# Kernel optimization log

Measured on AMD Instinct MI355X. Metric: run time of the kernel, lower is better.

The kernel has to match this reference:

```python
import jax, jax.numpy as jnp
import numpy as np

PRE_NMS_THRESH = 0.05
PRE_NMS_TOP_N = 1000
NMS_THRESH = 0.6
POST_TOP_N = 100
MIN_SIZE = 0.0


def setup_inputs() -> dict:
    key = jax.random.key(0)
    k1, k2, k3 = jax.random.split(key, 3)
    N, C, H, W = 16, 80, 100, 152
    stride = 8.0
    xs = (jnp.arange(W, dtype=jnp.float32) + 0.5) * stride
    ys = (jnp.arange(H, dtype=jnp.float32) + 0.5) * stride
    yy, xx = jnp.meshgrid(ys, xs, indexing='ij')
    locations = jnp.stack([xx.reshape(-1), yy.reshape(-1)], axis=-1)  # [HW,2] (x,y)
    box_cls = jax.random.normal(k1, (N, C, H, W), jnp.float32) - 2.0  # logits
    box_regression = jax.random.uniform(k2, (N, 4, H, W), jnp.float32) * 64.0  # l,t,r,b >= 0
    centerness = jax.random.normal(k3, (N, 1, H, W), jnp.float32)
    image_sizes = jnp.tile(jnp.array([[800, 1216]], dtype=jnp.int32), (N, 1))  # (h, w)
    return {"locations": locations, "box_cls": box_cls, "box_regression": box_regression,
            "centerness": centerness, "image_sizes": image_sizes}


def _iou_matrix(b):  # b: [K,4] xyxy
    area = (b[:, 2] - b[:, 0]) * (b[:, 3] - b[:, 1])
    lt = jnp.maximum(b[:, None, :2], b[None, :, :2])
    rb = jnp.minimum(b[:, None, 2:], b[None, :, 2:])
    wh = jnp.clip(rb - lt, 0.0)
    inter = wh[..., 0] * wh[..., 1]
    return inter / (area[:, None] + area[None, :] - inter + 1e-9)


def _greedy_nms(iou, valid):  # boxes assumed sorted by score desc
    K = iou.shape[0]
    idx = jnp.arange(K)
    def body(i, sup):
        row = (iou[i] > NMS_THRESH) & (idx > i)
        return jnp.where(sup[i], sup, sup | row)
    sup = jax.lax.fori_loop(0, K, body, ~valid)
    return (~sup) & valid


def _forward(locations, box_cls, box_regression, centerness, image_sizes):
    N, C, H, W = box_cls.shape
    HW = H * W
    cls = jax.nn.sigmoid(jnp.transpose(box_cls, (0, 2, 3, 1)).reshape(N, HW, C))
    reg = jnp.transpose(box_regression, (0, 2, 3, 1)).reshape(N, HW, 4)
    ctr = jax.nn.sigmoid(jnp.transpose(centerness, (0, 2, 3, 1)).reshape(N, HW))
    cand = cls > PRE_NMS_THRESH
    scores = cls * ctr[:, :, None]
    flat = jnp.where(cand, scores, -jnp.inf).reshape(N, HW * C)
    top_scores, top_idx = jax.lax.top_k(flat, PRE_NMS_TOP_N)  # sorted desc
    loc_idx = top_idx // C
    labels = top_idx % C + 1
    valid = top_scores > -jnp.inf
    ar = jnp.arange(N)[:, None]
    reg_k = reg[ar, loc_idx]      # [N,K,4]
    loc_k = locations[loc_idx]    # [N,K,2]
    x1 = loc_k[..., 0] - reg_k[..., 0]
    y1 = loc_k[..., 1] - reg_k[..., 1]
    x2 = loc_k[..., 0] + reg_k[..., 2]
    y2 = loc_k[..., 1] + reg_k[..., 3]
    hi = image_sizes[:, 0:1].astype(x1.dtype)
    wi = image_sizes[:, 1:2].astype(x1.dtype)
    x1 = jnp.clip(x1, 0.0, wi - 1.0); x2 = jnp.clip(x2, 0.0, wi - 1.0)
    y1 = jnp.clip(y1, 0.0, hi - 1.0); y2 = jnp.clip(y2, 0.0, hi - 1.0)
    valid = valid & (x2 - x1 >= MIN_SIZE) & (y2 - y1 >= MIN_SIZE)
    sc = jnp.where(valid, jnp.sqrt(jnp.where(valid, top_scores, 1.0)), 0.0)
    boxes = jnp.stack([x1, y1, x2, y2], axis=-1)  # [N,K,4]
    # multi-class NMS: offset each class into a disjoint coordinate range
    off = labels.astype(x1.dtype) * (jnp.maximum(wi, hi) + 1.0)
    iou = jax.vmap(_iou_matrix)(boxes + off[..., None])  # [N,K,K]
    keep = jax.vmap(_greedy_nms)(iou, valid)
    fscores = jnp.where(keep, sc, -1.0)
    fs, fidx = jax.lax.top_k(fscores, POST_TOP_N)
    fvalid = fs >= 0.0
    boxes_f = boxes[ar, fidx] * fvalid[..., None]
    labels_f = jnp.where(fvalid, labels[ar, fidx], 0)
    dets = jnp.concatenate([boxes_f, jnp.where(fvalid, fs, 0.0)[..., None]], axis=-1)  # [N,100,5]
    return dets, labels_f


def reference(locations, box_cls, box_regression, centerness, image_sizes):
    return _forward(locations, box_cls, box_regression, centerness, image_sizes)
```

## Files before the change

### kernel.cpp

```cpp
#include <hip/hip_runtime.h>
#include <cstdint>

#define NIMG  16
#define NCLS  80
#define HH    100
#define WW    152
#define HWSZ  (HH*WW)
#define HW4   (HWSZ/4)
#define NE    (HWSZ*NCLS)
#define KTOP  1000
#define POSTN 100
#define PRE_T 0.05f
#define NMS_T 0.6f
#define FLOOR_KEY 0x3D000000u
#define FLOOR_BIN 976
#define SEL_CAP   2048
#define NTILE 240
#define NCHUNK (NCLS*NTILE)
#define NSL1  20
#define NSL2  8
#define SCAP  2048
#define MSLICE 16

#define OFF_H1S   0u
#define OFF_H2S   2621440u
#define OFF_CANDS 3670016u
#define OFF_CCNT  5767168u
#define OFF_CMAX  5767680u
#define OFF_BOX   6996480u
#define OFF_SC    7252480u
#define OFF_LAB   7316480u
#define OFF_MASK  7380480u
#define OFF_COLS  9428480u
#define OFF_META  9559552u

__device__ __forceinline__ float sigm(float x) { return 1.f / (1.f + expf(-x)); }

__device__ __forceinline__ uint64_t shfl64(uint64_t v, int src) {
  int lo = __shfl((int)(uint32_t)(v & 0xffffffffu), src, 64);
  int hi = __shfl((int)(uint32_t)(v >> 32), src, 64);
  return ((uint64_t)(uint32_t)hi << 32) | (uint32_t)lo;
}
__device__ __forceinline__ uint64_t shfl64x(uint64_t v, int d) {
  int lo = __shfl_xor((int)(uint32_t)(v & 0xffffffffu), d, 64);
  int hi = __shfl_xor((int)(uint32_t)(v >> 32), d, 64);
  return ((uint64_t)(uint32_t)hi << 32) | (uint32_t)lo;
}

__device__ __forceinline__ void bitonic_desc_tpp(uint64_t* s, int nn, int t, int nt) {
  const int np = nn >> 1;
  for (int k2 = 2; k2 <= nn; k2 <<= 1) {
    for (int j = k2 >> 1; j > 0; j >>= 1) {
      __syncthreads();
      for (int q = t; q < np; q += nt) {
        int i = ((q & ~(j - 1)) << 1) | (q & (j - 1));
        int p = i | j;
        uint64_t a = s[i], b = s[p];
        bool desc = ((i & k2) == 0);
        bool sw = desc ? (a < b) : (a > b);
        if (sw) { s[i] = b; s[p] = a; }
      }
    }
  }
  __syncthreads();
}

__device__ __forceinline__ void findbin_par(
    const unsigned* __restrict__ hsum, unsigned K, int floorbin, int t,
    unsigned* wtot , int* binmax , unsigned* cumAb ,
    int* bin_out, unsigned* cumAbove_out) {
  const int lane = t & 63, w = t >> 6;
  const unsigned b0 = hsum[4 * t + 0], b1 = hsum[4 * t + 1];
  const unsigned b2 = hsum[4 * t + 2], b3 = hsum[4 * t + 3];
  unsigned s = b0 + b1 + b2 + b3;
#pragma unroll
  for (int d = 1; d < 64; d <<= 1) {
    unsigned o = (unsigned)__shfl_down((int)s, d, 64);
    if (lane + d < 64) s += o;
  }
  if (lane == 0) wtot[w] = s;
  if (t == 0) *binmax = -1;
  __syncthreads();
  unsigned wafter = 0;
#pragma unroll
  for (int w2 = 1; w2 < 16; ++w2) if (w + w2 < 16) wafter += wtot[w + w2];
  const unsigned s0 = s + wafter;
  const unsigned s1 = s0 - b0;
  const unsigned s2 = s1 - b1;
  const unsigned s3 = s2 - b2;
  int cand = -1;
  if (s3 >= K) cand = 4 * t + 3;
  else if (s2 >= K) cand = 4 * t + 2;
  else if (s1 >= K) cand = 4 * t + 1;
  else if (s0 >= K) cand = 4 * t + 0;
  if (cand >= 0) atomicMax(binmax, cand);
  __syncthreads();
  const int bin = *binmax;
  const int target = (bin >= 0) ? bin : floorbin;
  if (t == (target >> 2)) {
    unsigned suf = ((target & 3) == 0) ? s0 : ((target & 3) == 1) ? s1
                 : ((target & 3) == 2) ? s2 : s3;
    *cumAb = suf - hsum[target];
  }
  __syncthreads();
  *bin_out = target;
  *cumAbove_out = *cumAb;
}

__global__ void __launch_bounds__(1024) k_hist(
    const float4* __restrict__ cls4, const float4* __restrict__ ctr4,
    unsigned short* __restrict__ h1s, unsigned* __restrict__ cmax) {
  __shared__ unsigned h[4096];
  const int n = blockIdx.x, z = blockIdx.y;
  const int t = threadIdx.x;
  for (int i = t; i < 4096; i += 1024) h[i] = 0;
  __syncthreads();
  const float4* cp = cls4 + (size_t)n * (NE / 4);
  const float4* cr = ctr4 + (size_t)n * HW4;
#pragma unroll
  for (int it = 0; it < 4; ++it) {
    const int idx4 = it * 1024 + t;
    const bool val = idx4 < HW4;
    float ct0 = 0, ct1 = 0, ct2 = 0, ct3 = 0;
    if (val) {
      float4 c4 = cr[idx4];
      ct0 = sigm(c4.x); ct1 = sigm(c4.y); ct2 = sigm(c4.z); ct3 = sigm(c4.w);
    }
    const int tile = idx4 >> 4;
    for (int c = z * 4; c < z * 4 + 4; ++c) {
      unsigned k0 = 0, k1 = 0, k2 = 0, k3 = 0;
      if (val) {
        float4 v = cp[c * HW4 + idx4];
        float s0 = sigm(v.x), s1 = sigm(v.y), s2 = sigm(v.z), s3 = sigm(v.w);
        k0 = (s0 > PRE_T) ? __float_as_uint(s0 * ct0) : 0u;
        k1 = (s1 > PRE_T) ? __float_as_uint(s1 * ct1) : 0u;
        k2 = (s2 > PRE_T) ? __float_as_uint(s2 * ct2) : 0u;
        k3 = (s3 > PRE_T) ? __float_as_uint(s3 * ct3) : 0u;
        if (k0 >= FLOOR_KEY) atomicAdd(&h[k0 >> 20], 1u);
        if (k1 >= FLOOR_KEY) atomicAdd(&h[k1 >> 20], 1u);
        if (k2 >= FLOOR_KEY) atomicAdd(&h[k2 >> 20], 1u);
        if (k3 >= FLOOR_KEY) atomicAdd(&h[k3 >> 20], 1u);
      }
      unsigned km = max(max(k0, k1), max(k2, k3));
      km = max(km, (unsigned)__shfl_xor((int)km, 1, 64));
      km = max(km, (unsigned)__shfl_xor((int)km, 2, 64));
      km = max(km, (unsigned)__shfl_xor((int)km, 4, 64));
      km = max(km, (unsigned)__shfl_xor((int)km, 8, 64));
      if ((t & 15) == 0 && tile < NTILE)
        cmax[(size_t)n * NCHUNK + c * NTILE + tile] = km;
    }
  }
  __syncthreads();
  for (int i = t; i < 4096; i += 1024)
    h1s[(size_t)((n * NSL1 + z) << 12) + i] = (unsigned short)h[i];
}

__global__ void __launch_bounds__(1024) k_collect(
    const unsigned short* __restrict__ h1s, const unsigned* __restrict__ cmax,
    const float* __restrict__ cls, const float* __restrict__ ctr,
    uint64_t* __restrict__ candS, unsigned* __restrict__ ccnt,
    unsigned short* __restrict__ h2s, unsigned* __restrict__ meta) {
  __shared__ unsigned hsum[4096];
  __shared__ unsigned h2L[4096];
  __shared__ unsigned queue[2400];
  __shared__ unsigned wtot[16];
  __shared__ int binmax_s;
  __shared__ unsigned cumAb_s;
  __shared__ int qn_s, ccnt_s;
  const int s = blockIdx.x, n = blockIdx.y;
  const int t = threadIdx.x;
  for (int i = t; i < 4096; i += 1024) {
    unsigned v = 0;
    for (int z = 0; z < NSL1; ++z) v += (unsigned)h1s[(size_t)((n * NSL1 + z) << 12) + i];
    hsum[i] = v;
    h2L[i] = 0;
  }
  if (t == 0) { qn_s = 0; ccnt_s = 0; }
  __syncthreads();
  int bin1; unsigned cumAbove;
  findbin_par(hsum, (unsigned)KTOP, FLOOR_BIN, t, wtot, &binmax_s, &cumAb_s, &bin1, &cumAbove);
  if (s == 0 && t == 0) { meta[n * 16 + 0] = (unsigned)bin1; meta[n * 16 + 1] = cumAbove; }
  const unsigned thr1 = (unsigned)bin1, thrKey1 = thr1 << 20;
  const int c0 = s * (NCHUNK / NSL2);
  for (int i = t; i < NCHUNK / NSL2; i += 1024) {
    if (cmax[(size_t)n * NCHUNK + c0 + i] >= thrKey1) {
      int p = atomicAdd(&qn_s, 1);
      queue[p] = (unsigned)(c0 + i);
    }
  }
  __syncthreads();
  const int qn = qn_s;
  const int lane = t & 63, wv = t >> 6;
  for (int qi = wv; qi < qn; qi += 16) {
    int hc = (int)queue[qi];
    int c = hc / NTILE, tile = hc - c * NTILE;
    int hw = tile * 64 + lane;
    if (hw < HWSZ) {
      float s1 = sigm(cls[((size_t)n * NCLS + c) * HWSZ + hw]);
      float sc = sigm(ctr[(size_t)n * HWSZ + hw]);
      unsigned key = (s1 > PRE_T) ? __float_as_uint(s1 * sc) : 0u;
      if (key >= thrKey1) {
        unsigned fidx = (unsigned)(hw * NCLS + c);
        uint64_t comp = ((uint64_t)key << 21) | (uint64_t)(0x1FFFFFu - fidx);
        int p = atomicAdd(&ccnt_s, 1);
        if (p < SCAP) candS[(size_t)(n * NSL2 + s) * SCAP + p] = comp;
        if ((key >> 20) == thr1) atomicAdd(&h2L[(key >> 8) & 0xFFFu], 1u);
      }
    }
  }
  __syncthreads();
  for (int i = t; i < 4096; i += 1024)
    h2s[(size_t)((n * NSL2 + s) << 12) + i] = (unsigned short)h2L[i];
  if (t == 0) ccnt[n * NSL2 + s] = (unsigned)min(ccnt_s, SCAP);
}

__global__ void __launch_bounds__(1024) k_selmask(
    const unsigned short* __restrict__ h2s,
    const uint64_t* __restrict__ candS, const unsigned* __restrict__ ccnt,
    const float* __restrict__ locations, const float* __restrict__ breg,
    const int* __restrict__ imsz, unsigned* __restrict__ meta,
    float* __restrict__ boxes, float* __restrict__ scw, int* __restrict__ labw,
    uint64_t* __restrict__ masks, uint64_t* __restrict__ colsg) {
  __shared__ unsigned h2sum[4096];
  __shared__ uint64_t sel[SEL_CAP];
  __shared__ float4 obs[KTOP];
  __shared__ unsigned wtot[16];
  __shared__ int binmax_s;
  __shared__ unsigned cumAb_s;
  __shared__ int cnt2_s;
  const int slice = blockIdx.x, n = blockIdx.y;
  const int t = threadIdx.x;
  const int lane = t & 63, wv = t >> 6;
  const unsigned thr1 = meta[n * 16 + 0];
  const unsigned cumAbove = meta[n * 16 + 1];

  for (int i = t; i < 4096; i += 1024) {
    unsigned v2 = 0;
    for (int z = 0; z < NSL2; ++z) v2 += (unsigned)h2s[(size_t)((n * NSL2 + z) << 12) + i];
    h2sum[i] = v2;
  }
  if (t == 0) cnt2_s = 0;
  __syncthreads();
  int b2; unsigned dumCA;
  findbin_par(h2sum, (unsigned)((int)KTOP - (int)cumAbove), 0, t,
              wtot, &binmax_s, &cumAb_s, &b2, &dumCA);
  const unsigned thrKey2 = (thr1 << 20) | ((unsigned)b2 << 8);

  for (int s = 0; s < NSL2; ++s) {
    const int cn = (int)min(ccnt[n * NSL2 + s], (unsigned)SCAP);
    for (int j = t; j < cn; j += 1024) {
      uint64_t comp = candS[(size_t)(n * NSL2 + s) * SCAP + j];
      if ((unsigned)(comp >> 21) >= thrKey2) {
        int p = atomicAdd(&cnt2_s, 1);
        if (p < SEL_CAP) sel[p] = comp;
      }
    }
  }
  __syncthreads();
  const int m = min(cnt2_s, SEL_CAP);
  const int nn = (m <= 1024) ? 1024 : SEL_CAP;
  for (int j = m + t; j < nn; j += 1024) sel[j] = 0;
  __syncthreads();
  bitonic_desc_tpp(sel, nn, t, 1024);
  const int nv = min(m, KTOP);
  if (slice == 0 && t == 0) meta[n * 16 + 3] = (unsigned)nv;

  const float hi = (float)imsz[n * 2 + 0];
  const float wi = (float)imsz[n * 2 + 1];
  const float offmul = fmaxf(wi, hi) + 1.0f;
  if (t < KTOP) {
    const int k = t;
    float x1 = 0, y1 = 0, x2 = 0, y2 = 0, ox1 = 0, oy1 = 0, ox2 = 0, oy2 = 0, s = 0;
    int lab = 0;
    if (k < nv) {
      uint64_t comp = sel[k];
      unsigned key = (unsigned)(comp >> 21);
      unsigned idx = 0x1FFFFFu - (unsigned)(comp & 0x1FFFFFu);
      int hw = (int)(idx / NCLS);
      int c  = (int)(idx - (unsigned)hw * NCLS);
      lab = c + 1;
      float lx = locations[hw * 2 + 0];
      float ly = locations[hw * 2 + 1];
      const float* rg = breg + (size_t)n * 4 * HWSZ;
      float rl = rg[hw], rt = rg[HWSZ + hw], rr = rg[2 * HWSZ + hw], rb = rg[3 * HWSZ + hw];
      x1 = fminf(fmaxf(lx - rl, 0.f), wi - 1.f);
      x2 = fminf(fmaxf(lx + rr, 0.f), wi - 1.f);
      y1 = fminf(fmaxf(ly - rt, 0.f), hi - 1.f);
      y2 = fminf(fmaxf(ly + rb, 0.f), hi - 1.f);
      float off = (float)lab * offmul;
      asm volatile("" : "+v"(off));
      ox1 = x1 + off; oy1 = y1 + off; ox2 = x2 + off; oy2 = y2 + off;
      s = sqrtf(__uint_as_float(key));
    }
    if (slice == 0) {
      size_t bb = (size_t)(n * KTOP + k);
      boxes[bb * 4 + 0] = x1; boxes[bb * 4 + 1] = y1;
      boxes[bb * 4 + 2] = x2; boxes[bb * 4 + 3] = y2;
      scw[bb] = s;
      labw[bb] = lab;
    }
    obs[k] = make_float4(ox1, oy1, ox2, oy2);
  }
  __syncthreads();

  for (int rr = wv; rr < 63; rr += 16) {
    const int r = slice * 63 + rr;
    if (r >= nv) continue;
    const float4 bi = obs[r];
    float areai = (bi.z - bi.x) * (bi.w - bi.y);
    asm volatile("" : "+v"(areai));
    const int Wr = r >> 6;
    uint64_t* mr = masks + ((size_t)n * KTOP + r) * 16;
    for (int w = 0; w < 16; ++w) {
      int j = (w << 6) + lane;
      bool over = false;
      if (j < nv && j != r) {
        float4 bj = obs[j];
        float areaj = (bj.z - bj.x) * (bj.w - bj.y);
        asm volatile("" : "+v"(areaj));
        float ltx = fmaxf(bi.x, bj.x), lty = fmaxf(bi.y, bj.y);
        float rbx = fminf(bi.z, bj.z), rby = fminf(bi.w, bj.w);
        float wx = fmaxf(rbx - ltx, 0.f), wy = fmaxf(rby - lty, 0.f);
        float inter = wx * wy;
        asm volatile("" : "+v"(inter));
        float denom = areai + areaj - inter + 1e-9f;
        over = (inter / denom) > NMS_T;
      }
      uint64_t bu = __ballot(over && (j > r));
      if (lane == 0) mr[w] = bu;
      if (w == Wr) {
        uint64_t bc = __ballot(over && (j < r));
        if (lane == 0) colsg[((size_t)n * 16 + w) * 64 + (r & 63)] = bc;
      }
    }
  }
}

__global__ void __launch_bounds__(1024) k_scanout(
    const uint64_t* __restrict__ masks, const uint64_t* __restrict__ colsg,
    const unsigned* __restrict__ meta,
    const float* __restrict__ boxes, const float* __restrict__ scw,
    const int* __restrict__ labw, float* __restrict__ out) {
  __shared__ uint64_t shmP[KTOP * 17];
  __shared__ uint64_t keepb[16];
  const int n = blockIdx.x;
  const int t = threadIdx.x;
  const int lane = t & 63;
  const int nv = (int)meta[n * 16 + 3];
  const ulonglong2* src = (const ulonglong2*)(masks + (size_t)n * KTOP * 16);
  for (int j2 = t; j2 < KTOP * 8; j2 += 1024) {
    ulonglong2 v = src[j2];
    int row = j2 >> 3, wp = (j2 & 7) << 1;
    shmP[row * 17 + wp] = v.x;
    shmP[row * 17 + wp + 1] = v.y;
  }
  __syncthreads();
  if (t < 64) {
    uint64_t colr[16];
#pragma unroll
    for (int W = 0; W < 16; ++W) colr[W] = colsg[((size_t)n * 16 + W) * 64 + lane];
    uint64_t rmv = 0;
    const uint64_t below = (lane == 0) ? 0ull : (~0ull >> (64 - lane));
#pragma unroll
    for (int W = 0; W < 16; ++W) {
      const int lo = W << 6;
      uint64_t cur0 = shfl64(rmv, W);
      if (nv <= lo) cur0 = ~0ull;
      else if (nv < lo + 64) cur0 |= (~0ull) << (nv - lo);
      uint64_t kept = ~cur0;
      for (int it = 0; it < 64; ++it) {
        bool pred = (((cur0 >> lane) & 1ull) == 0) && ((colr[W] & kept & below) == 0ull);
        uint64_t kn = __ballot(pred);
        if (kn == kept) break;
        kept = kn;
      }
      if (lane == 0) keepb[W] = kept;
      const int w = lane & 15, g = lane >> 4;
      uint64_t acc = 0;
#pragma unroll
      for (int i2 = 0; i2 < 16; ++i2) {
        const int i = (i2 << 2) + g;
        uint64_t msk = (uint64_t)0 - ((kept >> i) & 1ull);
        acc |= shmP[(lo + i) * 17 + w] & msk;
      }
      acc |= shfl64x(acc, 16);
      acc |= shfl64x(acc, 32);
      if (lane < 16) rmv |= acc;
    }
  }
  __syncthreads();
  uint64_t* sel = shmP;
  {
    const int k = t;
    uint64_t comp = 0;
    if (k < KTOP && ((keepb[k >> 6] >> (k & 63)) & 1ull)) {
      unsigned s = __float_as_uint(scw[(size_t)n * KTOP + k]);
      comp = ((uint64_t)s << 10) | (uint64_t)(1023 - k);
    }
    sel[k] = comp;
  }
  __syncthreads();
  bitonic_desc_tpp(sel, 1024, t, 1024);
  if (t < POSTN) {
    const int k = t;
    uint64_t comp = sel[k];
    float x1 = 0, y1 = 0, x2 = 0, y2 = 0, fs = 0;
    int lab = 0;
    if (comp != 0) {
      int i = 1023 - (int)(comp & 0x3FFull);
      fs = __uint_as_float((unsigned)(comp >> 10));
      size_t bb = (size_t)(n * KTOP + i);
      x1 = boxes[bb * 4 + 0]; y1 = boxes[bb * 4 + 1];
      x2 = boxes[bb * 4 + 2]; y2 = boxes[bb * 4 + 3];
      lab = labw[bb];
    }
    float* dr = out + (size_t)(n * POSTN + k) * 5;
    dr[0] = x1; dr[1] = y1; dr[2] = x2; dr[3] = y2; dr[4] = fs;
    out[(size_t)NIMG * POSTN * 5 + (size_t)n * POSTN + k] = (float)lab;
  }
}

extern "C" void kernel_launch(void* const* d_in, const int* in_sizes, int n_in,
                              void* d_out, int out_size, void* d_ws, size_t ws_size,
                              hipStream_t stream) {
  const float* locations = (const float*)d_in[0];
  const float* box_cls = (const float*)d_in[1];
  const float* box_reg = (const float*)d_in[2];
  const float* centerness = (const float*)d_in[3];
  const int* image_sizes = (const int*)d_in[4];
  char* ws = (char*)d_ws;

  unsigned short* h1s = (unsigned short*)(ws + OFF_H1S);
  unsigned short* h2s = (unsigned short*)(ws + OFF_H2S);
  uint64_t* candS = (uint64_t*)(ws + OFF_CANDS);
  unsigned* ccnt = (unsigned*)(ws + OFF_CCNT);
  unsigned* cmaxp = (unsigned*)(ws + OFF_CMAX);
  float* boxes = (float*)(ws + OFF_BOX);
  float* scw = (float*)(ws + OFF_SC);
  int* labw = (int*)(ws + OFF_LAB);
  uint64_t* masks = (uint64_t*)(ws + OFF_MASK);
  uint64_t* colsg = (uint64_t*)(ws + OFF_COLS);
  unsigned* meta = (unsigned*)(ws + OFF_META);
  float* out = (float*)d_out;

  k_hist<<<dim3(NIMG, NSL1), 1024, 0, stream>>>((const float4*)box_cls,
                                                (const float4*)centerness, h1s, cmaxp);
  k_collect<<<dim3(NSL2, NIMG), 1024, 0, stream>>>(h1s, cmaxp, box_cls, centerness,
                                                   candS, ccnt, h2s, meta);
  k_selmask<<<dim3(MSLICE, NIMG), 1024, 0, stream>>>(h2s, candS, ccnt,
                                                     locations, box_reg, image_sizes, meta,
                                                     boxes, scw, labw, masks, colsg);
  k_scanout<<<NIMG, 1024, 0, stream>>>(masks, colsg, meta, boxes, scw, labw, out);
}
```

Before: 131.0 us.

## Stream NMS mask rows per block instead of staging all masks in LDS

The scan-out kernel no longer copies the full 1000x16 suppression mask matrix into shared memory up front. For each 64-box block it now reads only that block's 64 mask rows directly from global memory across all 1024 threads and ORs them into a shared removal vector with LDS atomics. This shrinks LDS use and removes the bulk prologue copy, but adds two block-wide barriers per block iteration (32 in total) and puts the global load latency on the serial critical path.

```diff
diff --git a/kernel.cpp b/kernel.cpp
--- a/kernel.cpp
+++ b/kernel.cpp
@@ -341,32 +341,35 @@
     const unsigned* __restrict__ meta,
     const float* __restrict__ boxes, const float* __restrict__ scw,
     const int* __restrict__ labw, float* __restrict__ out) {
-  __shared__ uint64_t shmP[KTOP * 17];
+  __shared__ uint64_t sel[1024];
   __shared__ uint64_t keepb[16];
+  __shared__ uint64_t rmvL[16];
+  __shared__ uint64_t keptS;
   const int n = blockIdx.x;
   const int t = threadIdx.x;
   const int lane = t & 63;
   const int nv = (int)meta[n * 16 + 3];
-  const ulonglong2* src = (const ulonglong2*)(masks + (size_t)n * KTOP * 16);
-  for (int j2 = t; j2 < KTOP * 8; j2 += 1024) {
-    ulonglong2 v = src[j2];
-    int row = j2 >> 3, wp = (j2 & 7) << 1;
-    shmP[row * 17 + wp] = v.x;
-    shmP[row * 17 + wp + 1] = v.y;
-  }
-  __syncthreads();
+  const uint64_t* mrow = masks + (size_t)n * KTOP * 16;
+
+  if (t < 16) {
+    int lo = t << 6;
+    uint64_t r = 0;
+    if (nv <= lo) r = ~0ull;
+    else if (nv < lo + 64) r = (~0ull) << (nv - lo);
+    rmvL[t] = r;
+  }
+  uint64_t colr[16];
   if (t < 64) {
-    uint64_t colr[16];
 #pragma unroll
     for (int W = 0; W < 16; ++W) colr[W] = colsg[((size_t)n * 16 + W) * 64 + lane];
-    uint64_t rmv = 0;
-    const uint64_t below = (lane == 0) ? 0ull : (~0ull >> (64 - lane));
-#pragma unroll
-    for (int W = 0; W < 16; ++W) {
-      const int lo = W << 6;
-      uint64_t cur0 = shfl64(rmv, W);
-      if (nv <= lo) cur0 = ~0ull;
-      else if (nv < lo + 64) cur0 |= (~0ull) << (nv - lo);
+  }
+  __syncthreads();
+
+  const int g = t >> 4, w = t & 15;
+  for (int W = 0; W < 16; ++W) {
+    if (t < 64) {
+      uint64_t cur0 = rmvL[W];
+      const uint64_t below = (lane == 0) ? 0ull : (~0ull >> (64 - lane));
       uint64_t kept = ~cur0;
       for (int it = 0; it < 64; ++it) {
         bool pred = (((cur0 >> lane) & 1ull) == 0) && ((colr[W] & kept & below) == 0ull);
@@ -374,22 +377,20 @@
         if (kn == kept) break;
         kept = kn;
       }
-      if (lane == 0) keepb[W] = kept;
-      const int w = lane & 15, g = lane >> 4;
-      uint64_t acc = 0;
-#pragma unroll
-      for (int i2 = 0; i2 < 16; ++i2) {
-        const int i = (i2 << 2) + g;
-        uint64_t msk = (uint64_t)0 - ((kept >> i) & 1ull);
-        acc |= shmP[(lo + i) * 17 + w] & msk;
-      }
+      if (lane == 0) { keptS = kept; keepb[W] = kept; }
+    }
+    __syncthreads();
+    {
+      const uint64_t kept = keptS;
+      uint64_t mv = mrow[(size_t)((W << 6) + g) * 16 + w];
+      uint64_t acc = mv & ((uint64_t)0 - ((kept >> g) & 1ull));
       acc |= shfl64x(acc, 16);
       acc |= shfl64x(acc, 32);
-      if (lane < 16) rmv |= acc;
-    }
-  }
-  __syncthreads();
-  uint64_t* sel = shmP;
+      if (lane < 16) atomicOr((unsigned long long*)&rmvL[w], (unsigned long long)acc);
+    }
+    __syncthreads();
+  }
+
   {
     const int k = t;
     uint64_t comp = 0;
```

After: 133.6 us. Within noise of the previous version (+2.0%).
